# Kernel optimization log

Measured on AMD Instinct MI355X. Metric: run time of the kernel, lower is better.

Reference implementation:

```python
import jax, jax.numpy as jnp
import numpy as np
from jax import lax

T = 8192
D_MODEL = 768
D_RNN = 1024
KW = 4  # conv kernel width


def setup_inputs() -> dict:
    key = jax.random.key(0)
    ks = jax.random.split(key, 9)
    x = jax.random.normal(ks[0], (T, D_MODEL), jnp.float32)
    # equinox nn.Linear(in, out): weight [out, in], bias [out]
    w1 = jax.random.normal(ks[1], (2 * D_RNN, D_MODEL), jnp.float32) / np.sqrt(D_MODEL)
    b1 = jnp.zeros((2 * D_RNN,), jnp.float32)
    # nn.Conv1d(d_rnn, d_rnn, 4, use_bias=False): kernel [out_ch, in_ch, kw]
    conv_w = jax.random.normal(ks[2], (D_RNN, D_RNN, KW), jnp.float32) / np.sqrt(D_RNN * KW)
    w_rg = jax.random.normal(ks[3], (2 * D_RNN, D_RNN), jnp.float32) / np.sqrt(D_RNN)
    b_rg = jnp.zeros((2 * D_RNN,), jnp.float32)
    w_out = jax.random.normal(ks[4], (D_MODEL, D_RNN), jnp.float32) / np.sqrt(D_RNN)
    b_out = jnp.zeros((D_MODEL,), jnp.float32)
    # Lambda ~ U(inv_sigmoid(0.9)^{1/8}, inv_sigmoid(0.999)^{1/8}) as in __init__
    inv_sig = lambda p: np.log(1.0 / (1.0 - p))
    lower = np.power(inv_sig(0.9), 1.0 / 8.0)
    upper = np.power(inv_sig(0.999), 1.0 / 8.0)
    Lambda = jax.random.uniform(ks[5], (D_RNN,), jnp.float32, lower, upper)
    return {"x": x, "w1": w1, "b1": b1, "conv_w": conv_w, "w_rg": w_rg,
            "b_rg": b_rg, "w_out": w_out, "b_out": b_out, "Lambda": Lambda}


def _rglru_forward(x, w1, b1, conv_w, w_rg, b_rg, w_out, b_out, Lambda):
    # lin1 then split into gate branch (gelu) and recurrent branch
    h = x @ w1.T + b1                       # [T, 2*D_RNN]
    a_branch = jax.nn.gelu(h[:, :D_RNN])    # [T, D_RNN]
    b_branch = h[:, D_RNN:]                 # [T, D_RNN]
    # causal conv1d: lhs [N=1, C, T], rhs [O, I, KW], left pad 3
    bc = lax.conv_general_dilated(b_branch.T[None], conv_w, (1,), [(KW - 1, 0)])[0].T  # [T, D_RNN]
    # RG-LRU gating
    g = jax.nn.sigmoid(bc @ w_rg.T + b_rg)  # [T, 2*D_RNN]
    inp_gate = g[:, :D_RNN]
    rec_gate = g[:, D_RNN:]
    a_t = jnp.exp(-8.0 * jax.nn.softplus(Lambda)[None, :] * rec_gate)  # [T, D_RNN]
    gated_x = jnp.sqrt(1.0 - a_t ** 2) * inp_gate * bc

    def rec_step(state, xs):
        gx, av = xs
        hn = av * state + gx
        return hn, hn

    _, y = lax.scan(rec_step, jnp.zeros((D_RNN,), x.dtype), (gated_x, a_t))
    return (a_branch * y) @ w_out.T + b_out  # [T, D_MODEL]


def reference(x, w1, b1, conv_w, w_rg, b_rg, w_out, b_out, Lambda):
    return _rglru_forward(x, w1, b1, conv_w, w_rg, b_rg, w_out, b_out, Lambda)
```

## Files before the change

### kernel.cpp

```cpp
#include <hip/hip_runtime.h>
#include <hip/hip_bf16.h>
#include <stdint.h>


#define T_LEN 8192
#define DM 768
#define DR 1024
#define NC 128
#define CL 64

typedef __bf16 bf16x8 __attribute__((ext_vector_type(8)));
typedef float  f32x4  __attribute__((ext_vector_type(4)));

#define AS1 __attribute__((address_space(1)))
#define AS3 __attribute__((address_space(3)))

__device__ __forceinline__ void cp16_g2l(const void* g, void* l) {
    __builtin_amdgcn_global_load_lds((const AS1 void*)g, (AS3 void*)l, 16, 0, 0);
}

__device__ __forceinline__ float gelu_tanh(float x) {
    const float inner = 0.7978845608028654f * (x + 0.044715f * x * x * x);
    return 0.5f * x * (1.f + tanhf(inner));
}

__device__ __forceinline__ __bf16 f2b(float v) {
    __hip_bfloat16 h = __float2bfloat16(v);
    return *reinterpret_cast<__bf16*>(&h);
}

template<int BN, int EPI, bool SHIFT>
__global__ __launch_bounds__(256, 4)
void gemm_mfma(const __hip_bfloat16* __restrict__ A,
               const __hip_bfloat16* __restrict__ B,
               const float* __restrict__ bias,
               void* __restrict__ Cv,
               int K, int lda, int N,
               __hip_bfloat16* __restrict__ D2)
{
    constexpr int NI  = BN / 32;
    constexpr int BLD = (BN * 4) / 256;
    constexpr int NLD = 2 + BLD;
    __shared__ __align__(16) unsigned char smem[32768];
    __bf16* Asb = (__bf16*)smem;
    __bf16* Bsb = (__bf16*)(smem + 16384);

    const int tid  = threadIdx.x;
    const int lane = tid & 63;
    const int wave = tid >> 6;
    const size_t m0 = (size_t)blockIdx.x * 128;
    const int    n0 = blockIdx.y * BN;
    const int wm = (wave >> 1) * 64;
    const int wn = (wave & 1) * (BN / 2);

    f32x4 acc[4][NI];
#pragma unroll
    for (int i = 0; i < 4; ++i)
#pragma unroll
        for (int j = 0; j < NI; ++j)
            acc[i][j] = f32x4{0.f, 0.f, 0.f, 0.f};

    const int frow = lane & 15;
    const int fq   = lane >> 4;

    auto stage = [&](int buf, int k0) {
#pragma unroll
        for (int q = 0; q < 2; ++q) {
            const int lin = q * 256 + tid;
            const int rr  = lin >> 2;
            const int gc  = (lin & 3) ^ ((rr >> 1) & 3);
            const size_t ar = m0 + rr + (SHIFT ? (size_t)(k0 >> 10) : 0);
            const int    ac = SHIFT ? (k0 & 1023) : k0;
            cp16_g2l(A + ar * (size_t)lda + ac + gc * 8, Asb + buf * 4096 + lin * 8);
        }
#pragma unroll
        for (int q = 0; q < BLD; ++q) {
            const int lin = q * 256 + tid;
            const int rr  = lin >> 2;
            const int gc  = (lin & 3) ^ ((rr >> 1) & 3);
            cp16_g2l(B + (size_t)(n0 + rr) * K + k0 + gc * 8,
                     Bsb + buf * (BN * 32) + lin * 8);
        }
    };

    const int nt = K / 32;
    stage(0, 0);
    int cur = 0;
    for (int t = 0; t < nt; ++t) {
        if (t + 1 < nt) {
            stage(cur ^ 1, (t + 1) * 32);
            asm volatile("s_waitcnt vmcnt(%0)" :: "n"(NLD) : "memory");
        } else {
            asm volatile("s_waitcnt vmcnt(0)" ::: "memory");
        }
        __builtin_amdgcn_sched_barrier(0);
        __builtin_amdgcn_s_barrier();
        __builtin_amdgcn_sched_barrier(0);

        bf16x8 af[4], bfr[NI];
#pragma unroll
        for (int mi = 0; mi < 4; ++mi) {
            const int R = wm + mi * 16 + frow;
            af[mi] = *(const bf16x8*)&Asb[cur * 4096 + R * 32 + ((fq ^ ((R >> 1) & 3)) * 8)];
        }
#pragma unroll
        for (int ni = 0; ni < NI; ++ni) {
            const int R = wn + ni * 16 + frow;
            bfr[ni] = *(const bf16x8*)&Bsb[cur * (BN * 32) + R * 32 + ((fq ^ ((R >> 1) & 3)) * 8)];
        }
        asm volatile("s_waitcnt lgkmcnt(0)" ::: "memory");
        __builtin_amdgcn_sched_barrier(0);
        __builtin_amdgcn_s_barrier();
        __builtin_amdgcn_sched_barrier(0);

        __builtin_amdgcn_s_setprio(1);
#pragma unroll
        for (int mi = 0; mi < 4; ++mi)
#pragma unroll
            for (int ni = 0; ni < NI; ++ni)
                acc[mi][ni] = __builtin_amdgcn_mfma_f32_16x16x32_bf16(
                    af[mi], bfr[ni], acc[mi][ni], 0, 0, 0);
        __builtin_amdgcn_s_setprio(0);
        cur ^= 1;
    }

    __syncthreads();
    const int er = fq * 4;
    const int ec = frow;

    if (EPI == 0) {
        float* Cl = (float*)smem;
#pragma unroll
        for (int ni = 0; ni < NI; ++ni) {
            const int cc = wn + ni * 16 + ec;
            const float bv = bias ? bias[n0 + cc] : 0.f;
#pragma unroll
            for (int mi = 0; mi < 4; ++mi)
#pragma unroll
                for (int r2 = 0; r2 < 4; ++r2) {
                    const int R = wm + mi * 16 + er + r2;
                    Cl[R * 64 + ((((cc >> 2) ^ (R & 7)) << 2) | (cc & 3))] =
                        acc[mi][ni][r2] + bv;
                }
        }
        __syncthreads();
        float* outp = (float*)Cv;
#pragma unroll
        for (int p = 0; p < 8; ++p) {
            const int R   = (tid >> 4) + p * 16;
            const int chn = tid & 15;
            const f32x4 v = *(const f32x4*)&Cl[R * 64 + ((chn ^ (R & 7)) << 2)];
            *(f32x4*)&outp[(m0 + R) * (size_t)N + n0 + chn * 4] = v;
        }
    } else {
        __bf16* Cl = (__bf16*)smem;
        const bool ahalf = (EPI == 2) && (n0 < 1024);
#pragma unroll
        for (int ni = 0; ni < NI; ++ni) {
            const int cc = wn + ni * 16 + ec;
            const float bv = bias ? bias[n0 + cc] : 0.f;
#pragma unroll
            for (int mi = 0; mi < 4; ++mi)
#pragma unroll
                for (int r2 = 0; r2 < 4; ++r2) {
                    const int R = wm + mi * 16 + er + r2;
                    float v = acc[mi][ni][r2] + bv;
                    if (EPI == 2 && ahalf) v = gelu_tanh(v);
                    Cl[R * 128 + ((((cc >> 3) ^ (R & 7)) << 3) | (cc & 7))] = f2b(v);
                }
        }
        __syncthreads();
#pragma unroll
        for (int p = 0; p < 8; ++p) {
            const int R   = (tid >> 4) + p * 16;
            const int chn = tid & 15;
            const bf16x8 v = *(const bf16x8*)&Cl[R * 128 + ((chn ^ (R & 7)) << 3)];
            if (EPI == 1) {
                *(bf16x8*)((__bf16*)Cv + (m0 + R) * (size_t)N + n0 + chn * 8) = v;
            } else if (n0 < 1024) {
                *(bf16x8*)((__bf16*)Cv + (m0 + R) * 1024 + n0 + chn * 8) = v;
            } else {
                *(bf16x8*)((__bf16*)D2 + (m0 + R + 3) * 1024 + (n0 - 1024) + chn * 8) = v;
            }
        }
    }
}

__global__ __launch_bounds__(256, 4)
void conv_mfma(const __hip_bfloat16* __restrict__ bbp,
               const __hip_bfloat16* __restrict__ W,
               __hip_bfloat16* __restrict__ C)
{
    __shared__ __align__(16) unsigned char smem[33280];
    __bf16* Ah = (__bf16*)smem;
    __bf16* Bt = (__bf16*)(smem + 16896);

    const int tid  = threadIdx.x;
    const int lane = tid & 63;
    const int wave = tid >> 6;
    const size_t m0 = (size_t)blockIdx.x * 128;
    const int    n0 = blockIdx.y * 128;
    const int wm = (wave >> 1) * 64;
    const int wn = (wave & 1) * 64;

    f32x4 acc[4][4];
#pragma unroll
    for (int i = 0; i < 4; ++i)
#pragma unroll
        for (int j = 0; j < 4; ++j)
            acc[i][j] = f32x4{0.f, 0.f, 0.f, 0.f};

    const int frow = lane & 15;
    const int fq   = lane >> 4;

    auto stageA = [&](int abuf, int kc) {
#pragma unroll
        for (int q = 0; q < 2; ++q) {
            const int lin = q * 256 + tid;
            const int rr  = lin >> 2;
            const int gc  = (lin & 3) ^ ((rr >> 1) & 3);
            cp16_g2l(bbp + (m0 + rr) * 1024 + kc + gc * 8, Ah + abuf * 4224 + lin * 8);
        }
        if (tid < 16) {
            const int lin = 512 + tid;
            const int rr  = lin >> 2;
            const int gc  = (lin & 3) ^ ((rr >> 1) & 3);
            cp16_g2l(bbp + (m0 + rr) * 1024 + kc + gc * 8, Ah + abuf * 4224 + lin * 8);
        }
    };
    auto stageB = [&](int bbuf, int u) {
        const int s  = u & 3;
        const int kc = (u >> 2) * 32;
#pragma unroll
        for (int q = 0; q < 2; ++q) {
            const int lin = q * 256 + tid;
            const int rr  = lin >> 2;
            const int gc  = (lin & 3) ^ ((rr >> 1) & 3);
            cp16_g2l(W + (size_t)(n0 + rr) * 4096 + s * 1024 + kc + gc * 8,
                     Bt + bbuf * 4096 + lin * 8);
        }
    };

    stageA(0, 0);
    stageB(0, 0);
    int acur = 0, bcur = 0;
    for (int u = 0; u < 128; ++u) {
        const int s = u & 3;
        if (u + 1 < 128) {
            stageB(bcur ^ 1, u + 1);
            if (s == 3) {
                stageA(acur ^ 1, ((u >> 2) + 1) * 32);
                asm volatile("s_waitcnt vmcnt(4)" ::: "memory");
            } else {
                asm volatile("s_waitcnt vmcnt(2)" ::: "memory");
            }
        } else {
            asm volatile("s_waitcnt vmcnt(0)" ::: "memory");
        }
        __builtin_amdgcn_sched_barrier(0);
        __builtin_amdgcn_s_barrier();
        __builtin_amdgcn_sched_barrier(0);

        bf16x8 af[4], bfr[4];
#pragma unroll
        for (int mi = 0; mi < 4; ++mi) {
            const int R = wm + mi * 16 + frow + s;
            af[mi] = *(const bf16x8*)&Ah[acur * 4224 + R * 32 + ((fq ^ ((R >> 1) & 3)) * 8)];
        }
#pragma unroll
        for (int ni = 0; ni < 4; ++ni) {
            const int R = wn + ni * 16 + frow;
            bfr[ni] = *(const bf16x8*)&Bt[bcur * 4096 + R * 32 + ((fq ^ ((R >> 1) & 3)) * 8)];
        }
        asm volatile("s_waitcnt lgkmcnt(0)" ::: "memory");
        __builtin_amdgcn_sched_barrier(0);
        __builtin_amdgcn_s_barrier();
        __builtin_amdgcn_sched_barrier(0);

        __builtin_amdgcn_s_setprio(1);
#pragma unroll
        for (int mi = 0; mi < 4; ++mi)
#pragma unroll
            for (int ni = 0; ni < 4; ++ni)
                acc[mi][ni] = __builtin_amdgcn_mfma_f32_16x16x32_bf16(
                    af[mi], bfr[ni], acc[mi][ni], 0, 0, 0);
        __builtin_amdgcn_s_setprio(0);

        bcur ^= 1;
        if (s == 3) acur ^= 1;
    }

    __syncthreads();
    const int er = fq * 4;
    const int ec = frow;
    __bf16* Cl = (__bf16*)smem;
#pragma unroll
    for (int ni = 0; ni < 4; ++ni) {
        const int cc = wn + ni * 16 + ec;
#pragma unroll
        for (int mi = 0; mi < 4; ++mi)
#pragma unroll
            for (int r2 = 0; r2 < 4; ++r2) {
                const int R = wm + mi * 16 + er + r2;
                Cl[R * 128 + ((((cc >> 3) ^ (R & 7)) << 3) | (cc & 7))] =
                    f2b(acc[mi][ni][r2]);
            }
    }
    __syncthreads();
#pragma unroll
    for (int p = 0; p < 8; ++p) {
        const int R   = (tid >> 4) + p * 16;
        const int chn = tid & 15;
        const bf16x8 v = *(const bf16x8*)&Cl[R * 128 + ((chn ^ (R & 7)) << 3)];
        *(bf16x8*)((__bf16*)C + (m0 + R) * 1024 + n0 + chn * 8) = v;
    }
}

#define PREP_X   6291456
#define PREP_W1  (PREP_X + 1572864)
#define PREP_WRG (PREP_W1 + 2097152)
#define PREP_WO  (PREP_WRG + 786432)
#define PREP_CW  (PREP_WO + 4194304)
#define PREP_TOT (PREP_CW + 3072)
__global__ void prep_kernel(const float* __restrict__ x, const float* __restrict__ w1,
                            const float* __restrict__ w_rg, const float* __restrict__ w_out,
                            const float* __restrict__ conv_w,
                            __hip_bfloat16* __restrict__ xb, __hip_bfloat16* __restrict__ w1b,
                            __hip_bfloat16* __restrict__ w_rgb, __hip_bfloat16* __restrict__ w_outb,
                            __hip_bfloat16* __restrict__ wbigb, __hip_bfloat16* __restrict__ bbp)
{
    const int idx = blockIdx.x * 256 + threadIdx.x;
    if (idx < PREP_X) {
        xb[idx] = __float2bfloat16(x[idx]);
    } else if (idx < PREP_W1) {
        const int i = idx - PREP_X;  w1b[i] = __float2bfloat16(w1[i]);
    } else if (idx < PREP_WRG) {
        const int i = idx - PREP_W1; w_rgb[i] = __float2bfloat16(w_rg[i]);
    } else if (idx < PREP_WO) {
        const int i = idx - PREP_WRG; w_outb[i] = __float2bfloat16(w_out[i]);
    } else if (idx < PREP_CW) {
        const int n = idx - PREP_WO;
        const int o = n >> 12, r = n & 4095, k = r >> 10, i = r & 1023;
        wbigb[n] = __float2bfloat16(conv_w[o * 4096 + i * 4 + k]);
    } else {
        bbp[idx - PREP_CW] = __float2bfloat16(0.f);
    }
}

__global__ void scan_pass1(const __hip_bfloat16* __restrict__ gp,
                           const __hip_bfloat16* __restrict__ bc,
                           const float* __restrict__ Lambda,
                           float* __restrict__ ch, float* __restrict__ ca)
{
    const int c = blockIdx.y * 256 + threadIdx.x;
    const int j = blockIdx.x;
    const float cl = -8.f * log1pf(expf(Lambda[c]));
    float h = 0.f, ap = 1.f;
    const int t0 = j * CL;
    for (int tt = 0; tt < CL; ++tt) {
        const int t = t0 + tt;
        const long gi = (long)t * 2048 + c;
        const float ig = 1.f / (1.f + expf(-__bfloat162float(gp[gi])));
        const float rg = 1.f / (1.f + expf(-__bfloat162float(gp[gi + 1024])));
        const float a  = expf(cl * rg);
        const float gx = sqrtf(fmaxf(0.f, 1.f - a * a)) * ig *
                         __bfloat162float(bc[(long)t * 1024 + c]);
        h  = fmaf(a, h, gx);
        ap *= a;
    }
    ch[j * 1024 + c] = h;
    ca[j * 1024 + c] = ap;
}

__global__ void scan_combine(float* __restrict__ ch, const float* __restrict__ ca)
{
    const int c = blockIdx.x * 256 + threadIdx.x;
    float carry = 0.f;
    for (int j = 0; j < NC; ++j) {
        const float hj = ch[j * 1024 + c];
        const float aj = ca[j * 1024 + c];
        ch[j * 1024 + c] = carry;
        carry = fmaf(aj, carry, hj);
    }
}

__global__ void scan_pass2(const __hip_bfloat16* __restrict__ gp, const __hip_bfloat16* bc,
                           const float* __restrict__ Lambda,
                           const float* __restrict__ carry_in,
                           const __hip_bfloat16* __restrict__ ab,
                           __hip_bfloat16* zb)
{
    const int c = blockIdx.y * 256 + threadIdx.x;
    const int j = blockIdx.x;
    const float cl = -8.f * log1pf(expf(Lambda[c]));
    float h = carry_in[j * 1024 + c];
    const int t0 = j * CL;
    for (int tt = 0; tt < CL; ++tt) {
        const int t = t0 + tt;
        const long gi = (long)t * 2048 + c;
        const long bi = (long)t * 1024 + c;
        const float ig = 1.f / (1.f + expf(-__bfloat162float(gp[gi])));
        const float rg = 1.f / (1.f + expf(-__bfloat162float(gp[gi + 1024])));
        const float a  = expf(cl * rg);
        const float gx = sqrtf(fmaxf(0.f, 1.f - a * a)) * ig * __bfloat162float(bc[bi]);
        h = fmaf(a, h, gx);
        zb[bi] = __float2bfloat16(__bfloat162float(ab[bi]) * h);
    }
}

extern "C" void kernel_launch(void* const* d_in, const int* in_sizes, int n_in,
                              void* d_out, int out_size, void* d_ws, size_t ws_size,
                              hipStream_t stream)
{
    const float* x      = (const float*)d_in[0];
    const float* w1     = (const float*)d_in[1];
    const float* b1     = (const float*)d_in[2];
    const float* conv_w = (const float*)d_in[3];
    const float* w_rg   = (const float*)d_in[4];
    const float* b_rg   = (const float*)d_in[5];
    const float* w_out  = (const float*)d_in[6];
    const float* b_out  = (const float*)d_in[7];
    const float* Lambda = (const float*)d_in[8];
    float* out = (float*)d_out;
    (void)in_sizes; (void)n_in; (void)out_size; (void)ws_size;

    char* p = (char*)d_ws;
    auto alloc = [&](size_t bytes) { char* r = p; p += (bytes + 255) & ~255ULL; return r; };
    __hip_bfloat16* gpre  = (__hip_bfloat16*)alloc(8192ULL * 2048 * 2);
    __hip_bfloat16* ab    = (__hip_bfloat16*)alloc(8192ULL * 1024 * 2);
    __hip_bfloat16* bbp   = (__hip_bfloat16*)alloc(8200ULL * 1024 * 2);
    __hip_bfloat16* bcb   = (__hip_bfloat16*)alloc(8192ULL * 1024 * 2);
    __hip_bfloat16* wbigb = (__hip_bfloat16*)alloc(1024ULL * 4096 * 2);
    __hip_bfloat16* xb    = (__hip_bfloat16*)alloc(8192ULL * 768 * 2);
    __hip_bfloat16* w1b   = (__hip_bfloat16*)alloc(2048ULL * 768 * 2);
    __hip_bfloat16* w_rgb = (__hip_bfloat16*)alloc(2048ULL * 1024 * 2);
    __hip_bfloat16* w_outb= (__hip_bfloat16*)alloc(768ULL * 1024 * 2);
    float*          chv   = (float*)alloc(NC * 1024ULL * 4);
    float*          cav   = (float*)alloc(NC * 1024ULL * 4);
    __hip_bfloat16* zb    = bcb;

    prep_kernel<<<PREP_TOT / 256, 256, 0, stream>>>(x, w1, w_rg, w_out, conv_w,
                                                    xb, w1b, w_rgb, w_outb, wbigb, bbp);

    {
        dim3 grid(T_LEN / 128, 2048 / 128);
        gemm_mfma<128, 2, false><<<grid, 256, 0, stream>>>(xb, w1b, b1, ab, DM, DM, 2048, bbp);
    }

    {
        dim3 grid(T_LEN / 128, 1024 / 128);
        conv_mfma<<<grid, 256, 0, stream>>>(bbp, wbigb, bcb);
    }

    {
        dim3 grid(T_LEN / 128, 2048 / 128);
        gemm_mfma<128, 1, false><<<grid, 256, 0, stream>>>(bcb, w_rgb, b_rg, gpre, DR, DR, 2048, nullptr);
    }

    {
        dim3 gs(NC, DR / 256);
        scan_pass1<<<gs, 256, 0, stream>>>(gpre, bcb, Lambda, chv, cav);
        scan_combine<<<DR / 256, 256, 0, stream>>>(chv, cav);
        scan_pass2<<<gs, 256, 0, stream>>>(gpre, bcb, Lambda, chv, ab, zb);
    }

    {
        dim3 grid(T_LEN / 128, DM / 64);
        gemm_mfma<64, 0, false><<<grid, 256, 0, stream>>>(zb, w_outb, b_out, out, DR, DR, DM, nullptr);
    }
}
```

Measured before the change: 273.3 us.

## Stage all four conv taps per K-chunk in conv GEMM pipeline

```diff
diff --git a/kernel.cpp b/kernel.cpp
--- a/kernel.cpp
+++ b/kernel.cpp
@@ -186,14 +186,14 @@
     }
 }
 
-__global__ __launch_bounds__(256, 4)
+__global__ __launch_bounds__(256, 2)
 void conv_mfma(const __hip_bfloat16* __restrict__ bbp,
                const __hip_bfloat16* __restrict__ W,
                __hip_bfloat16* __restrict__ C)
 {
-    __shared__ __align__(16) unsigned char smem[33280];
+    __shared__ __align__(16) unsigned char smem[73984];
     __bf16* Ah = (__bf16*)smem;
-    __bf16* Bt = (__bf16*)(smem + 16896);
+    __bf16* Bt = (__bf16*)(smem + 8448);
 
     const int tid  = threadIdx.x;
     const int lane = tid & 63;
@@ -213,47 +213,41 @@
     const int frow = lane & 15;
     const int fq   = lane >> 4;
 
-    auto stageA = [&](int abuf, int kc) {
+    auto stageA = [&](int kc) {
 #pragma unroll
         for (int q = 0; q < 2; ++q) {
             const int lin = q * 256 + tid;
             const int rr  = lin >> 2;
             const int gc  = (lin & 3) ^ ((rr >> 1) & 3);
-            cp16_g2l(bbp + (m0 + rr) * 1024 + kc + gc * 8, Ah + abuf * 4224 + lin * 8);
+            cp16_g2l(bbp + (m0 + rr) * 1024 + kc + gc * 8, Ah + lin * 8);
         }
         if (tid < 16) {
             const int lin = 512 + tid;
             const int rr  = lin >> 2;
             const int gc  = (lin & 3) ^ ((rr >> 1) & 3);
-            cp16_g2l(bbp + (m0 + rr) * 1024 + kc + gc * 8, Ah + abuf * 4224 + lin * 8);
+            cp16_g2l(bbp + (m0 + rr) * 1024 + kc + gc * 8, Ah + lin * 8);
         }
     };
-    auto stageB = [&](int bbuf, int u) {
-        const int s  = u & 3;
-        const int kc = (u >> 2) * 32;
-#pragma unroll
-        for (int q = 0; q < 2; ++q) {
-            const int lin = q * 256 + tid;
-            const int rr  = lin >> 2;
-            const int gc  = (lin & 3) ^ ((rr >> 1) & 3);
-            cp16_g2l(W + (size_t)(n0 + rr) * 4096 + s * 1024 + kc + gc * 8,
-                     Bt + bbuf * 4096 + lin * 8);
-        }
+    auto stageB = [&](int buf, int kc) {
+#pragma unroll
+        for (int s = 0; s < 4; ++s)
+#pragma unroll
+            for (int q = 0; q < 2; ++q) {
+                const int lin = q * 256 + tid;
+                const int rr  = lin >> 2;
+                const int gc  = (lin & 3) ^ ((rr >> 1) & 3);
+                cp16_g2l(W + (size_t)(n0 + rr) * 4096 + s * 1024 + kc + gc * 8,
+                         Bt + buf * 16384 + s * 4096 + lin * 8);
+            }
     };
 
-    stageA(0, 0);
+    stageA(0);
     stageB(0, 0);
-    int acur = 0, bcur = 0;
-    for (int u = 0; u < 128; ++u) {
-        const int s = u & 3;
-        if (u + 1 < 128) {
-            stageB(bcur ^ 1, u + 1);
-            if (s == 3) {
-                stageA(acur ^ 1, ((u >> 2) + 1) * 32);
-                asm volatile("s_waitcnt vmcnt(4)" ::: "memory");
-            } else {
-                asm volatile("s_waitcnt vmcnt(2)" ::: "memory");
-            }
+    int bcur = 0;
+    for (int t = 0; t < 32; ++t) {
+        if (t + 1 < 32) {
+            stageB(bcur ^ 1, (t + 1) * 32);
+            asm volatile("s_waitcnt vmcnt(8)" ::: "memory");
         } else {
             asm volatile("s_waitcnt vmcnt(0)" ::: "memory");
         }
@@ -261,33 +255,34 @@
         __builtin_amdgcn_s_barrier();
         __builtin_amdgcn_sched_barrier(0);
 
-        bf16x8 af[4], bfr[4];
-#pragma unroll
-        for (int mi = 0; mi < 4; ++mi) {
-            const int R = wm + mi * 16 + frow + s;
-            af[mi] = *(const bf16x8*)&Ah[acur * 4224 + R * 32 + ((fq ^ ((R >> 1) & 3)) * 8)];
-        }
-#pragma unroll
-        for (int ni = 0; ni < 4; ++ni) {
-            const int R = wn + ni * 16 + frow;
-            bfr[ni] = *(const bf16x8*)&Bt[bcur * 4096 + R * 32 + ((fq ^ ((R >> 1) & 3)) * 8)];
-        }
-        asm volatile("s_waitcnt lgkmcnt(0)" ::: "memory");
+        __builtin_amdgcn_s_setprio(1);
+#pragma unroll
+        for (int s = 0; s < 4; ++s) {
+            bf16x8 af[4], bfr[4];
+#pragma unroll
+            for (int mi = 0; mi < 4; ++mi) {
+                const int R = wm + mi * 16 + frow + s;
+                af[mi] = *(const bf16x8*)&Ah[R * 32 + ((fq ^ ((R >> 1) & 3)) * 8)];
+            }
+#pragma unroll
+            for (int ni = 0; ni < 4; ++ni) {
+                const int R = wn + ni * 16 + frow;
+                bfr[ni] = *(const bf16x8*)&Bt[bcur * 16384 + s * 4096 + R * 32 +
+                                              ((fq ^ ((R >> 1) & 3)) * 8)];
+            }
+#pragma unroll
+            for (int mi = 0; mi < 4; ++mi)
+#pragma unroll
+                for (int ni = 0; ni < 4; ++ni)
+                    acc[mi][ni] = __builtin_amdgcn_mfma_f32_16x16x32_bf16(
+                        af[mi], bfr[ni], acc[mi][ni], 0, 0, 0);
+        }
+        __builtin_amdgcn_s_setprio(0);
         __builtin_amdgcn_sched_barrier(0);
         __builtin_amdgcn_s_barrier();
         __builtin_amdgcn_sched_barrier(0);
-
-        __builtin_amdgcn_s_setprio(1);
-#pragma unroll
-        for (int mi = 0; mi < 4; ++mi)
-#pragma unroll
-            for (int ni = 0; ni < 4; ++ni)
-                acc[mi][ni] = __builtin_amdgcn_mfma_f32_16x16x32_bf16(
-                    af[mi], bfr[ni], acc[mi][ni], 0, 0, 0);
-        __builtin_amdgcn_s_setprio(0);
-
+        if (t + 1 < 32) stageA((t + 1) * 32);
         bcur ^= 1;
-        if (s == 3) acur ^= 1;
     }
 
     __syncthreads();
```

New measurement: 272.3 us (median of 2 runs). Within noise of the previous version (-0.4%).
